# Performance work log

Measured on AMD Instinct MI355X. Metric: run time of the kernel, lower is better.

## Reference

```python
import jax, jax.numpy as jnp
import numpy as np

B, S, V, NC, CV, CE, WE, KS = 64, 256, 50000, 20, 256, 32, 512, 4


def setup_inputs() -> dict:
    key = jax.random.key(0)
    k1, k2, k3, k4 = jax.random.split(key, 4)
    data = jax.random.randint(k1, (B, S), 0, V, dtype=jnp.int32)
    spelling = jax.random.randint(k2, (V, NC), 0, CV, dtype=jnp.int32)
    char_emb_w = jax.random.normal(k3, (CV, CE), dtype=jnp.float32)
    cnn_w = jax.random.uniform(k4, (WE, CE + 1, KS), dtype=jnp.float32,
                               minval=-0.05, maxval=0.05)
    return {"char_emb_w": char_emb_w, "cnn_w": cnn_w,
            "data": data, "spelling": spelling}


def reference(char_emb_w, cnn_w, data, spelling):
    # spelling gather: [B,S] -> [B,S,NC] char ids -> [B,S,NC,CE] char embeddings
    sp = spelling[data]
    ce = char_emb_w[sp]
    bsz, seq_len, nc, ces = ce.shape
    x = ce.reshape(bsz * seq_len, nc, ces)
    # mode='l2' -> lang bit is 1.0 (would be 0.0 for 'l1')
    lang_bit = jnp.ones((bsz * seq_len, nc, 1), dtype=x.dtype)
    x = jnp.concatenate([x, lang_bit], axis=2).transpose(0, 2, 1)  # [N, CE+1, NC]
    # Conv1d, valid padding, no bias: [N, WE, NC-KS+1]
    y = jax.lax.conv_general_dilated(x, cnn_w, window_strides=(1,),
                                     padding='VALID',
                                     dimension_numbers=('NCH', 'OIH', 'NCH'))
    # MaxPool1d over full remaining length
    word_emb = jnp.max(y, axis=2)  # [N, WE]
    return word_emb.reshape(bsz, seq_len, -1)
```

## Files before the change

kernel.cpp:

```cpp
#include <hip/hip_runtime.h>
#include <hip/hip_bf16.h>
#include <cstdint>

#define NWORDS 16384
#define NCH    20
#define CEDIM  32
#define WEDIM  512

typedef __attribute__((ext_vector_type(8)))  short bf16x8;
typedef __attribute__((ext_vector_type(16))) float f32x16;

__device__ __forceinline__ unsigned short f2bf(float f){
    union { float f; unsigned int u; } v; v.f = f;
    unsigned int u = v.u + 0x7fffu + ((v.u >> 16) & 1u);
    return (unsigned short)(u >> 16);
}

__global__ __launch_bounds__(256) void prep_kernel(const float* __restrict__ cnn,
                                                   const float* __restrict__ cemb,
                                                   unsigned short* __restrict__ wbf3,
                                                   unsigned short* __restrict__ cembbf,
                                                   float* __restrict__ bias){
    int idx = blockIdx.x * 256 + threadIdx.x;
    if (idx < 65536){
        int j   = idx & 7;
        int col = (idx >> 3) & 31;
        int lh  = (idx >> 8) & 1;
        int s   = (idx >> 9) & 7;
        int cc  = idx >> 12;
        int o   = cc*32 + col;
        int kk  = s*16 + lh*8 + j;
        int i   = kk & 31, k = kk >> 5;
        wbf3[idx] = f2bf(cnn[o*132 + i*4 + k]);
    } else if (idx < 65536 + 256*CEDIM){
        int r = idx - 65536;
        cembbf[r] = f2bf(cemb[r]);
    } else if (idx < 65536 + 256*CEDIM + WEDIM){
        int o = idx - (65536 + 256*CEDIM);
        const float* p = cnn + o*132 + 128;
        bias[o] = p[0] + p[1] + p[2] + p[3];
    }
}

__global__ __attribute__((amdgpu_waves_per_eu(2))) __launch_bounds__(128)
void conv_kernel(
    const int* __restrict__ data,
    const int* __restrict__ spelling,
    const unsigned short* __restrict__ cembbf,
    const unsigned short* __restrict__ wbf3,
    const float* __restrict__ bias,
    float* __restrict__ out)
{
    const int tid  = threadIdx.x;
    const int wv   = tid >> 6;
    const int lane = tid & 63;
    const int ln31 = lane & 31;
    const int lh   = lane >> 5;
    const int wgrp = blockIdx.x >> 2;
    const int cg   = blockIdx.x & 3;
    const int wbase = wgrp * 32;

    int wd = data[wbase + ln31];
    const int4* sp = reinterpret_cast<const int4*>(spelling + wd*NCH);
    int4 s0 = sp[0], s1 = sp[1], s2 = sp[2], s3 = sp[3], s4 = sp[4];
    unsigned idpk[5];
    idpk[0] = (unsigned)s0.x | ((unsigned)s0.y<<8) | ((unsigned)s0.z<<16) | ((unsigned)s0.w<<24);
    idpk[1] = (unsigned)s1.x | ((unsigned)s1.y<<8) | ((unsigned)s1.z<<16) | ((unsigned)s1.w<<24);
    idpk[2] = (unsigned)s2.x | ((unsigned)s2.y<<8) | ((unsigned)s2.z<<16) | ((unsigned)s2.w<<24);
    idpk[3] = (unsigned)s3.x | ((unsigned)s3.y<<8) | ((unsigned)s3.z<<16) | ((unsigned)s3.w<<24);
    idpk[4] = (unsigned)s4.x | ((unsigned)s4.y<<8) | ((unsigned)s4.z<<16) | ((unsigned)s4.w<<24);

    const char* cb = (const char*)cembbf;
    const char* wb = (const char*)wbf3;

    auto afrag = [&](int c, int p) -> bf16x8 {
        unsigned id = (idpk[c >> 2] >> ((c & 3)*8)) & 0xFFu;
        return *reinterpret_cast<const bf16x8*>(cb + id*64 + p*32 + lh*16);
    };

    f32x16 zz;
    #pragma unroll
    for (int r = 0; r < 16; ++r) zz[r] = 0.f;

    #pragma unroll 1
    for (int ch2 = 0; ch2 < 2; ++ch2){
        const int cc16 = cg*4 + wv*2 + ch2;
        const int colb = cc16*32;

        const char* wbb = wb + cc16*8192 + lane*16;
        bf16x8 bs[8];
        #pragma unroll
        for (int s = 0; s < 8; ++s)
            bs[s] = *reinterpret_cast<const bf16x8*>(wbb + s*1024);

        bf16x8 aw[4][2];
        #pragma unroll
        for (int c = 0; c < 4; ++c){
            aw[c][0] = afrag(c, 0);
            aw[c][1] = afrag(c, 1);
        }

        f32x16 vmax;
        #pragma unroll
        for (int t = 0; t < 17; ++t){
            f32x16 acc;
            acc = __builtin_amdgcn_mfma_f32_32x32x16_bf16(aw[ t   &3][0], bs[0], zz,  0,0,0);
            acc = __builtin_amdgcn_mfma_f32_32x32x16_bf16(aw[ t   &3][1], bs[1], acc, 0,0,0);
            acc = __builtin_amdgcn_mfma_f32_32x32x16_bf16(aw[(t+1)&3][0], bs[2], acc, 0,0,0);
            acc = __builtin_amdgcn_mfma_f32_32x32x16_bf16(aw[(t+1)&3][1], bs[3], acc, 0,0,0);
            acc = __builtin_amdgcn_mfma_f32_32x32x16_bf16(aw[(t+2)&3][0], bs[4], acc, 0,0,0);
            acc = __builtin_amdgcn_mfma_f32_32x32x16_bf16(aw[(t+2)&3][1], bs[5], acc, 0,0,0);
            acc = __builtin_amdgcn_mfma_f32_32x32x16_bf16(aw[(t+3)&3][0], bs[6], acc, 0,0,0);
            acc = __builtin_amdgcn_mfma_f32_32x32x16_bf16(aw[(t+3)&3][1], bs[7], acc, 0,0,0);

            if (t == 0){
                vmax = acc;
            } else {
                #pragma unroll
                for (int r = 0; r < 16; ++r) vmax[r] = fmaxf(vmax[r], acc[r]);
            }
            if (t < 16){
                aw[t&3][0] = afrag(t+4, 0);
                aw[t&3][1] = afrag(t+4, 1);
            }
        }

        float bv = bias[colb + ln31];
        #pragma unroll
        for (int r = 0; r < 16; ++r){
            int row = (r & 3) + 8*(r >> 2) + 4*lh;
            __builtin_nontemporal_store(vmax[r] + bv,
                out + (wbase + row)*WEDIM + colb + ln31);
        }
    }
}

extern "C" void kernel_launch(void* const* d_in, const int* in_sizes, int n_in,
                              void* d_out, int out_size, void* d_ws, size_t ws_size,
                              hipStream_t stream) {
    const float* cemb     = (const float*)d_in[0];
    const float* cnn      = (const float*)d_in[1];
    const int*   data     = (const int*)d_in[2];
    const int*   spelling = (const int*)d_in[3];
    float* outp = (float*)d_out;

    unsigned short* wbf3   = (unsigned short*)d_ws;
    float*          bias   = (float*)((char*)d_ws + 131072);
    unsigned short* cembbf = (unsigned short*)((char*)d_ws + 133120);

    int prep_items = 65536 + 256*CEDIM + WEDIM;
    prep_kernel<<<dim3((prep_items + 255)/256), dim3(256), 0, stream>>>(cnn, cemb, wbf3, cembbf, bias);
    conv_kernel<<<dim3(2048), dim3(128), 0, stream>>>(data, spelling, cembbf, wbf3, bias, outp);
}
```

Measured before the change: 104.8 us.

## Stage gathered char embeddings in LDS and cover all output columns per block

Each block now handles 32 words with 8 waves spanning all 512 output columns, instead of four blocks per word group each redoing the spelling gather. The bf16 character embeddings for the block's words are gathered once into shared memory, and MFMA A-fragments are then read from LDS. This removes the repeated global gather of spelling ids and embeddings across column groups. The cost is a __syncthreads, 40KB of LDS per block, and fewer, larger blocks (512 instead of 2048), which may lower occupancy and latency hiding.

```diff
diff --git a/kernel.cpp b/kernel.cpp
--- a/kernel.cpp
+++ b/kernel.cpp
@@ -6,6 +6,8 @@
 #define NCH    20
 #define CEDIM  32
 #define WEDIM  512
+#define WPB    32
+#define NBLK   (NWORDS/WPB)
 
 typedef __attribute__((ext_vector_type(8)))  short bf16x8;
 typedef __attribute__((ext_vector_type(16))) float f32x16;
@@ -42,7 +44,7 @@
     }
 }
 
-__global__ __attribute__((amdgpu_waves_per_eu(2))) __launch_bounds__(128)
+__global__ __attribute__((amdgpu_waves_per_eu(2))) __launch_bounds__(512)
 void conv_kernel(
     const int* __restrict__ data,
     const int* __restrict__ spelling,
@@ -51,31 +53,36 @@
     const float* __restrict__ bias,
     float* __restrict__ out)
 {
+    __shared__ __align__(16) char sA[20*4*32*16];
+
     const int tid  = threadIdx.x;
     const int wv   = tid >> 6;
     const int lane = tid & 63;
     const int ln31 = lane & 31;
     const int lh   = lane >> 5;
-    const int wgrp = blockIdx.x >> 2;
-    const int cg   = blockIdx.x & 3;
-    const int wbase = wgrp * 32;
+    const int wbase = blockIdx.x * WPB;
 
-    int wd = data[wbase + ln31];
-    const int4* sp = reinterpret_cast<const int4*>(spelling + wd*NCH);
-    int4 s0 = sp[0], s1 = sp[1], s2 = sp[2], s3 = sp[3], s4 = sp[4];
-    unsigned idpk[5];
-    idpk[0] = (unsigned)s0.x | ((unsigned)s0.y<<8) | ((unsigned)s0.z<<16) | ((unsigned)s0.w<<24);
-    idpk[1] = (unsigned)s1.x | ((unsigned)s1.y<<8) | ((unsigned)s1.z<<16) | ((unsigned)s1.w<<24);
-    idpk[2] = (unsigned)s2.x | ((unsigned)s2.y<<8) | ((unsigned)s2.z<<16) | ((unsigned)s2.w<<24);
-    idpk[3] = (unsigned)s3.x | ((unsigned)s3.y<<8) | ((unsigned)s3.z<<16) | ((unsigned)s3.w<<24);
-    idpk[4] = (unsigned)s4.x | ((unsigned)s4.y<<8) | ((unsigned)s4.z<<16) | ((unsigned)s4.w<<24);
+    {
+        auto stage = [&](int c, int w){
+            int wd = data[wbase + w];
+            int id = spelling[wd*NCH + c];
+            const uint4* src = reinterpret_cast<const uint4*>(cembbf + id*CEDIM);
+            #pragma unroll
+            for (int q = 0; q < 4; ++q){
+                uint4 v = src[q];
+                *reinterpret_cast<uint4*>(sA + ((c*4 + q) << 9) + (w << 4)) = v;
+            }
+        };
+        stage(tid >> 5, tid & 31);
+        if (tid < 128) stage(16 + (tid >> 5), tid & 31);
+    }
+    __syncthreads();
 
-    const char* cb = (const char*)cembbf;
     const char* wb = (const char*)wbf3;
 
-    auto afrag = [&](int c, int p) -> bf16x8 {
-        unsigned id = (idpk[c >> 2] >> ((c & 3)*8)) & 0xFFu;
-        return *reinterpret_cast<const bf16x8*>(cb + id*64 + p*32 + lh*16);
+    auto ldA = [&](int c, int p) -> bf16x8 {
+        return *reinterpret_cast<const bf16x8*>(
+            sA + ((c*4 + p*2 + lh) << 9) + (ln31 << 4));
     };
 
     f32x16 zz;
@@ -83,8 +90,8 @@
     for (int r = 0; r < 16; ++r) zz[r] = 0.f;
 
     #pragma unroll 1
-    for (int ch2 = 0; ch2 < 2; ++ch2){
-        const int cc16 = cg*4 + wv*2 + ch2;
+    for (int half = 0; half < 2; ++half){
+        const int cc16 = wv + half*8;
         const int colb = cc16*32;
 
         const char* wbb = wb + cc16*8192 + lane*16;
@@ -96,8 +103,8 @@
         bf16x8 aw[4][2];
         #pragma unroll
         for (int c = 0; c < 4; ++c){
-            aw[c][0] = afrag(c, 0);
-            aw[c][1] = afrag(c, 1);
+            aw[c][0] = ldA(c, 0);
+            aw[c][1] = ldA(c, 1);
         }
 
         f32x16 vmax;
@@ -120,8 +127,8 @@
                 for (int r = 0; r < 16; ++r) vmax[r] = fmaxf(vmax[r], acc[r]);
             }
             if (t < 16){
-                aw[t&3][0] = afrag(t+4, 0);
-                aw[t&3][1] = afrag(t+4, 1);
+                aw[t&3][0] = ldA(t+4, 0);
+                aw[t&3][1] = ldA(t+4, 1);
             }
         }
 
@@ -150,5 +157,5 @@
 
     int prep_items = 65536 + 256*CEDIM + WEDIM;
     prep_kernel<<<dim3((prep_items + 255)/256), dim3(256), 0, stream>>>(cnn, cemb, wbf3, cembbf, bias);
-    conv_kernel<<<dim3(2048), dim3(128), 0, stream>>>(data, spelling, cembbf, wbf3, bias, outp);
+    conv_kernel<<<dim3(NBLK), dim3(512), 0, stream>>>(data, spelling, cembbf, wbf3, bias, outp);
 }
```

Result: faster. 100.3 us (-4.2%).
